# Kernel tuning notes

Hardware: AMD Instinct MI355X
Metric: run time of the kernel (lower is better)

Reference implementation:

```python
import jax, jax.numpy as jnp
import numpy as np

V, D, C, H = 32, 128, 2048, 8
B, M = 8, 2048
HD = D // H


def rms_norm(x, scale):
    # Whole-tensor (per-batch) RMS over dims (1,2), as in the source (quirky but faithful).
    Bx, Mx, Dx = x.shape
    fr = jnp.sqrt(jnp.sum(x * x, axis=(1, 2))) * (Mx * Dx) ** -0.5  # (B,)
    raw = x / fr[:, None, None]
    return scale[:Mx, :][None, :, :] * raw


def rope_tables(Mx):
    i = jnp.arange(D // 2, dtype=jnp.float32)
    # NOTE: faithful to source: exponent uses (i-1), not i.
    base = jnp.power(10000.0, -2.0 * (i - 1.0) / D)  # (D/2,)
    pos = jnp.arange(Mx, dtype=jnp.float32)
    ang = pos[:, None] * base[None, :]  # (M, D/2)
    return jnp.cos(ang), jnp.sin(ang)


def apply_rope(t, cos, sin):
    # Equivalent to bmm with the block-diagonal 2x2 rotation matrices:
    # out[2i]   =  t[2i]*cos + t[2i+1]*sin
    # out[2i+1] = -t[2i]*sin + t[2i+1]*cos
    te, to = t[..., 0::2], t[..., 1::2]
    oe = te * cos + to * sin
    oo = -te * sin + to * cos
    return jnp.stack([oe, oo], axis=-1).reshape(t.shape)


def mha(q, k, v, in_w, in_b, out_w, out_b):
    Bx, Mx, _ = q.shape
    qp = q @ in_w[:D].T + in_b[:D]
    kp = k @ in_w[D:2 * D].T + in_b[D:2 * D]
    vp = v @ in_w[2 * D:].T + in_b[2 * D:]
    qh = qp.reshape(Bx, Mx, H, HD).transpose(0, 2, 1, 3)
    kh = kp.reshape(Bx, Mx, H, HD).transpose(0, 2, 1, 3)
    vh = vp.reshape(Bx, Mx, H, HD).transpose(0, 2, 1, 3)
    scores = jnp.einsum('bhqd,bhkd->bhqk', qh, kh) / jnp.sqrt(jnp.float32(HD))
    causal = jnp.tril(jnp.ones((Mx, Mx), dtype=bool))
    scores = jnp.where(causal[None, None], scores, -jnp.inf)
    probs = jax.nn.softmax(scores, axis=-1)  # dropout=0.1 in train mode; eval here
    o = jnp.einsum('bhqk,bhkd->bhqd', probs, vh)
    o = o.transpose(0, 2, 1, 3).reshape(Bx, Mx, D)
    return o @ out_w.T + out_b


def setup_inputs():
    key = jax.random.key(0)
    ks = jax.random.split(key, 12)
    s = 0.02
    return {
        'idx': jax.random.randint(ks[0], (B, M), 0, V),
        'targets': jax.random.randint(ks[1], (B, M), 0, V),
        'emb': jax.random.normal(ks[2], (V, D), jnp.float32) * s,
        'rms_scale': jnp.ones((C, D), jnp.float32),
        'Wq': jax.random.normal(ks[3], (D, D), jnp.float32) * s,
        'Wk': jax.random.normal(ks[4], (D, D), jnp.float32) * s,
        'Wv': jax.random.normal(ks[5], (D, D), jnp.float32) * s,
        'in_proj_w': jax.random.normal(ks[6], (3 * D, D), jnp.float32) * s,
        'in_proj_b': jnp.zeros((3 * D,), jnp.float32),
        'out_proj_w': jax.random.normal(ks[7], (D, D), jnp.float32) * s,
        'out_proj_b': jnp.zeros((D,), jnp.float32),
        'lin_w': jax.random.normal(ks[8], (D, D), jnp.float32) * s,
        'lin_b': jnp.zeros((D,), jnp.float32),
        'out_w': jax.random.normal(ks[9], (V, D), jnp.float32) * s,
        'out_b': jnp.zeros((V,), jnp.float32),
    }


def reference(idx, targets, emb, rms_scale, Wq, Wk, Wv, in_proj_w, in_proj_b,
              out_proj_w, out_proj_b, lin_w, lin_b, out_w, out_b):
    x = emb[idx]                                  # (B, M, D)
    x = rms_norm(x, rms_scale)
    Q = x @ Wq.T
    K = x @ Wk.T
    Vv = x @ Wv.T
    cos, sin = rope_tables(x.shape[1])
    q_out = apply_rope(Q, cos, sin)
    k_out = apply_rope(K, cos, sin)
    v_out = apply_rope(Vv, cos, sin)              # source rotates V too (faithful)
    x = x + mha(q_out, k_out, v_out, in_proj_w, in_proj_b, out_proj_w, out_proj_b)
    x = rms_norm(x, rms_scale)
    x = x + jax.nn.relu(x @ lin_w.T + lin_b)
    logits = x @ out_w.T + out_b                  # (B, M, V)
    logp = jax.nn.log_softmax(logits, axis=-1)
    nll = -jnp.take_along_axis(logp, targets[..., None], axis=-1)[..., 0]
    loss = jnp.mean(nll)
    return logits, loss
```

## Files before the change

### kernel.cpp

```cpp
#include <hip/hip_runtime.h>
#include <hip/hip_bf16.h>
#include <math.h>

#define Vv   32
#define Dd   128
#define Hh   8
#define Bb   8
#define Mm   2048
#define BM   (Bb*Mm)
#define NEL  (BM*Dd)
#define XNS  140
#define QKS  396

typedef _Float16 half4_t __attribute__((ext_vector_type(4)));
typedef _Float16 half8_t __attribute__((ext_vector_type(8)));
typedef __fp16   fp16x2  __attribute__((ext_vector_type(2)));
typedef float    float4_t __attribute__((ext_vector_type(4)));
#define MFMA16 __builtin_amdgcn_mfma_f32_16x16x16f16

#if __has_builtin(__builtin_amdgcn_exp2f)
__device__ __forceinline__ float fexp2(float x) { return __builtin_amdgcn_exp2f(x); }
#else
__device__ __forceinline__ float fexp2(float x) { return __expf(x * 0.6931471805599453f); }
#endif

__global__ __launch_bounds__(256) void prep_kernel(const float* __restrict__ Wq,
                                                   const float* __restrict__ Wk,
                                                   const float* __restrict__ Wv,
                                                   const float* __restrict__ in_w,
                                                   const float* __restrict__ out_pw,
                                                   const float* __restrict__ lin_w,
                                                   const float* __restrict__ out_w,
                                                   _Float16* __restrict__ Wh,
                                                   float* __restrict__ cosT,
                                                   float* __restrict__ sinT) {
    int gid = blockIdx.x * 256 + threadIdx.x;
    if (gid < 135168) {
        const float* src;
        int i;
        if (gid < 131072) {
            int seg = gid >> 14; i = gid & 16383;
            src = seg == 0 ? Wq : seg == 1 ? Wk : seg == 2 ? Wv :
                  seg < 6 ? in_w + (size_t)(seg - 3) * 16384 :
                  seg == 6 ? out_pw : lin_w;
        } else { src = out_w; i = gid - 131072; }
        int tile = i >> 8, within = i & 255;
        int nt = tile >> 3, kk = tile & 7;
        int r = within >> 4, cc = within & 15;
        Wh[gid] = (_Float16)src[(nt * 16 + r) * 128 + kk * 16 + cc];
    } else {
        int rid = gid - 135168;
        int i = rid & 63, m = rid >> 6;
        float ex = -2.0f * ((float)i - 1.0f) / 128.0f;
        float basef = expf(ex * 9.210340371976184f);
        float ang = (float)m * basef;
        cosT[rid] = cosf(ang);
        sinT[rid] = sinf(ang);
    }
}

__global__ __launch_bounds__(256) void gather_sumsq_kernel(const int* __restrict__ idx,
                                                           const float* __restrict__ emb,
                                                           _Float16* __restrict__ Xh,
                                                           float* __restrict__ partials) {
    int gid = blockIdx.x * 256 + threadIdx.x;
    int token = gid >> 5, t4 = gid & 31;
    float4 x = *(const float4*)(emb + (size_t)idx[token] * 128 + t4 * 4);
    half4_t o;
    o[0] = (_Float16)x.x; o[1] = (_Float16)x.y; o[2] = (_Float16)x.z; o[3] = (_Float16)x.w;
    *(half4_t*)(Xh + (size_t)gid * 4) = o;
    float v = x.x * x.x + x.y * x.y + x.z * x.z + x.w * x.w;
    #pragma unroll
    for (int off = 32; off; off >>= 1) v += __shfl_xor(v, off);
    __shared__ float wsum[4];
    int lane = threadIdx.x & 63, wave = threadIdx.x >> 6;
    if (lane == 0) wsum[wave] = v;
    __syncthreads();
    if (threadIdx.x == 0) partials[blockIdx.x] = wsum[0] + wsum[1] + wsum[2] + wsum[3];
}

__global__ __launch_bounds__(256) void normscale_f_kernel(const float* __restrict__ X,
                                                          const float* __restrict__ scale,
                                                          const float* __restrict__ part2,
                                                          _Float16* __restrict__ outh) {
    int gid = blockIdx.x * 256 + threadIdx.x;
    int b = gid >> 16;
    float pv = part2[b * 64 + (threadIdx.x & 63)];
    #pragma unroll
    for (int off = 32; off; off >>= 1) pv += __shfl_xor(pv, off);
    float iv = 512.0f / sqrtf(pv);
    const float* sp = scale + (size_t)((gid >> 5) & 2047) * 128 + (gid & 31) * 4;
    float4 s4 = *(const float4*)sp;
    float4 x = *(const float4*)(X + (size_t)gid * 4);
    half4_t o;
    o[0] = (_Float16)(x.x * iv * s4.x);
    o[1] = (_Float16)(x.y * iv * s4.y);
    o[2] = (_Float16)(x.z * iv * s4.z);
    o[3] = (_Float16)(x.w * iv * s4.w);
    *(half4_t*)(outh + (size_t)gid * 4) = o;
}

__global__ __launch_bounds__(256) void gemm_qkvproj_kernel(const _Float16* __restrict__ xh,
                                                           const float* __restrict__ scale,
                                                           const float* __restrict__ part1,
                                                           const _Float16* __restrict__ Whqkv,
                                                           const _Float16* __restrict__ Whin,
                                                           const float* __restrict__ in_b,
                                                           const float* __restrict__ cosT,
                                                           const float* __restrict__ sinT,
                                                           _Float16* __restrict__ xnh,
                                                           _Float16* __restrict__ Qp,
                                                           _Float16* __restrict__ Kp,
                                                           _Float16* __restrict__ Vp) {
    __shared__ _Float16 xn[32 * XNS];
    __shared__ _Float16 qkv[32 * QKS];
    __shared__ float wsum0[4];
    int tid = threadIdx.x;
    int row0 = blockIdx.x * 32;
    {
        float v = part1[(row0 >> 11) * 256 + tid];
        #pragma unroll
        for (int off = 32; off; off >>= 1) v += __shfl_xor(v, off);
        if ((tid & 63) == 0) wsum0[tid >> 6] = v;
    }
    __syncthreads();
    float iv = 512.0f / sqrtf(wsum0[0] + wsum0[1] + wsum0[2] + wsum0[3]);
    {
        #pragma unroll
        for (int it = 0; it < 2; it++) {
            int idx = tid + it * 256;
            int rw = idx >> 4, c8 = (idx & 15) * 8;
            int m = (row0 + rw) & (Mm - 1);
            half8_t x8 = *(const half8_t*)(xh + (size_t)(row0 + rw) * 128 + c8);
            const float* sp = scale + (size_t)m * 128 + c8;
            float4 s0 = *(const float4*)sp;
            float4 s1 = *(const float4*)(sp + 4);
            half8_t o8;
            o8[0] = (_Float16)((float)x8[0] * iv * s0.x);
            o8[1] = (_Float16)((float)x8[1] * iv * s0.y);
            o8[2] = (_Float16)((float)x8[2] * iv * s0.z);
            o8[3] = (_Float16)((float)x8[3] * iv * s0.w);
            o8[4] = (_Float16)((float)x8[4] * iv * s1.x);
            o8[5] = (_Float16)((float)x8[5] * iv * s1.y);
            o8[6] = (_Float16)((float)x8[6] * iv * s1.z);
            o8[7] = (_Float16)((float)x8[7] * iv * s1.w);
            *(half8_t*)(xn + rw * XNS + c8) = o8;
            *(half8_t*)(xnh + (size_t)(row0 + rw) * 128 + c8) = o8;
        }
    }
    __syncthreads();
    int wave = tid >> 6, lane = tid & 63;
    int r = lane & 15, c = lane >> 4;
    int lofs = r * 16 + 4 * c;
    int nb = wave * 96;
    int nb16 = wave * 6;
    {
        half4_t af[2][8];
        #pragma unroll
        for (int rt = 0; rt < 2; rt++)
            #pragma unroll
            for (int kk = 0; kk < 8; kk++)
                af[rt][kk] = *(const half4_t*)(xn + (rt * 16 + r) * XNS + kk * 16 + 4 * c);
        float4_t acc[2][6];
        #pragma unroll
        for (int rt = 0; rt < 2; rt++)
            #pragma unroll
            for (int t = 0; t < 6; t++) acc[rt][t] = (float4_t){0.f, 0.f, 0.f, 0.f};
        #pragma unroll
        for (int kk = 0; kk < 8; kk++) {
            half4_t wf[6];
            #pragma unroll
            for (int t = 0; t < 6; t++)
                wf[t] = *(const half4_t*)(Whqkv + ((nb16 + t) * 8 + kk) * 256 + lofs);
            #pragma unroll
            for (int t = 0; t < 6; t++) {
                acc[0][t] = MFMA16(af[0][kk], wf[t], acc[0][t], 0, 0, 0);
                acc[1][t] = MFMA16(af[1][kk], wf[t], acc[1][t], 0, 0, 0);
            }
        }
        #pragma unroll
        for (int rt = 0; rt < 2; rt++) {
            #pragma unroll
            for (int t = 0; t < 6; t++) {
                int n = nb + t * 16 + r;
                int ci = (n & 127) >> 1;
                #pragma unroll
                for (int reg = 0; reg < 4; reg++) {
                    int m2 = (row0 + rt * 16 + 4 * c + reg) & (Mm - 1);
                    float v = acc[rt][t][reg];
                    float vp = __shfl_xor(v, 1);
                    float cs = cosT[m2 * 64 + ci], sn = sinT[m2 * 64 + ci];
                    v = (n & 1) ? (-vp * sn + v * cs) : (v * cs + vp * sn);
                    qkv[(rt * 16 + 4 * c + reg) * QKS + n] = (_Float16)v;
                }
            }
        }
    }
    __syncthreads();
    {
        int seg_lo = nb >> 7;
        int seg_hi = (nb + 80) >> 7;
        half4_t aql[2][8], aqh[2][8];
        #pragma unroll
        for (int rt = 0; rt < 2; rt++)
            #pragma unroll
            for (int kk = 0; kk < 8; kk++) {
                aql[rt][kk] = *(const half4_t*)(qkv + (rt * 16 + r) * QKS + seg_lo * 128 + kk * 16 + 4 * c);
                aqh[rt][kk] = *(const half4_t*)(qkv + (rt * 16 + r) * QKS + seg_hi * 128 + kk * 16 + 4 * c);
            }
        float4_t acc[2][6];
        #pragma unroll
        for (int rt = 0; rt < 2; rt++)
            #pragma unroll
            for (int t = 0; t < 6; t++) acc[rt][t] = (float4_t){0.f, 0.f, 0.f, 0.f};
        #pragma unroll
        for (int kk = 0; kk < 8; kk++) {
            half4_t wf[6];
            #pragma unroll
            for (int t = 0; t < 6; t++) {
                int colg = nb + t * 16;
                int seg = colg >> 7;
                int ntl = (colg & 127) >> 4;
                wf[t] = *(const half4_t*)(Whin + ((seg * 8 + ntl) * 8 + kk) * 256 + lofs);
            }
            #pragma unroll
            for (int t = 0; t < 6; t++) {
                int seg = (nb + t * 16) >> 7;
                acc[0][t] = MFMA16(seg == seg_lo ? aql[0][kk] : aqh[0][kk], wf[t], acc[0][t], 0, 0, 0);
                acc[1][t] = MFMA16(seg == seg_lo ? aql[1][kk] : aqh[1][kk], wf[t], acc[1][t], 0, 0, 0);
            }
        }
        int bb = row0 >> 11;
        #pragma unroll
        for (int rt = 0; rt < 2; rt++) {
            int t16 = ((row0 + rt * 16) & 2047) >> 4;
            #pragma unroll
            for (int t = 0; t < 6; t++) {
                int colg = nb + t * 16;
                int seg = colg >> 7;
                int h = (colg & 127) >> 4;
                size_t tb = ((size_t)(bb * 8 + h) * 128 + t16) * 256;
                float bv = in_b[colg + r];
                _Float16* dst = seg == 0 ? Qp : seg == 1 ? Kp : Vp;
                #pragma unroll
                for (int reg = 0; reg < 4; reg++) {
                    float v = acc[rt][t][reg] + bv;
                    int key = 4 * c + reg;
                    if (seg < 2) dst[tb + key * 16 + r] = (_Float16)v;
                    else         dst[tb + r * 16 + key] = (_Float16)v;
                }
            }
        }
    }
}

__global__ __launch_bounds__(256) void gemm_ep1_kernel(const _Float16* __restrict__ Oh,
                                                       const _Float16* __restrict__ W6,
                                                       const float* __restrict__ bias,
                                                       const _Float16* __restrict__ xnh,
                                                       float* __restrict__ xres,
                                                       float* __restrict__ partials) {
    __shared__ _Float16 At[32 * XNS];
    int tid = threadIdx.x;
    int row0 = blockIdx.x * 32;
    #pragma unroll
    for (int it = 0; it < 2; it++) {
        int idx = tid + it * 256;
        int rw = idx >> 4, c8 = (idx & 15) * 8;
        *(half8_t*)(At + rw * XNS + c8) = *(const half8_t*)(Oh + (size_t)(row0 + rw) * 128 + c8);
    }
    __syncthreads();
    int wave = tid >> 6, lane = tid & 63;
    int r = lane & 15, c = lane >> 4;
    int lofs = r * 16 + 4 * c;
    int n0 = wave * 32;
    half4_t af[2][8];
    #pragma unroll
    for (int rt = 0; rt < 2; rt++)
        #pragma unroll
        for (int kk = 0; kk < 8; kk++)
            af[rt][kk] = *(const half4_t*)(At + (rt * 16 + r) * XNS + kk * 16 + 4 * c);
    float4_t acc[2][2];
    #pragma unroll
    for (int rt = 0; rt < 2; rt++) {
        acc[rt][0] = (float4_t){0.f, 0.f, 0.f, 0.f};
        acc[rt][1] = (float4_t){0.f, 0.f, 0.f, 0.f};
    }
    #pragma unroll
    for (int kk = 0; kk < 8; kk++) {
        half4_t wf[2];
        wf[0] = *(const half4_t*)(W6 + ((wave * 2 + 0) * 8 + kk) * 256 + lofs);
        wf[1] = *(const half4_t*)(W6 + ((wave * 2 + 1) * 8 + kk) * 256 + lofs);
        #pragma unroll
        for (int t = 0; t < 2; t++) {
            acc[0][t] = MFMA16(af[0][kk], wf[t], acc[0][t], 0, 0, 0);
            acc[1][t] = MFMA16(af[1][kk], wf[t], acc[1][t], 0, 0, 0);
        }
    }
    float lssq = 0.f;
    #pragma unroll
    for (int rt = 0; rt < 2; rt++) {
        #pragma unroll
        for (int t = 0; t < 2; t++) {
            int n = n0 + t * 16 + r;
            float bv = bias[n];
            #pragma unroll
            for (int reg = 0; reg < 4; reg++) {
                int row = row0 + rt * 16 + 4 * c + reg;
                float v = acc[rt][t][reg] + bv + (float)xnh[(size_t)row * 128 + n];
                lssq += v * v;
                xres[(size_t)row * 128 + n] = v;
            }
        }
    }
    #pragma unroll
    for (int off = 32; off; off >>= 1) lssq += __shfl_xor(lssq, off);
    __shared__ float wsum[4];
    if (lane == 0) wsum[wave] = lssq;
    __syncthreads();
    if (tid == 0) partials[blockIdx.x] = wsum[0] + wsum[1] + wsum[2] + wsum[3];
}

__global__ __launch_bounds__(256) void gemm_ep2_kernel(const _Float16* __restrict__ Ah,
                                                       const _Float16* __restrict__ W7,
                                                       const float* __restrict__ bias,
                                                       const float* __restrict__ xres,
                                                       _Float16* __restrict__ ffoh) {
    __shared__ _Float16 At[32 * XNS];
    int tid = threadIdx.x;
    int row0 = blockIdx.x * 32;
    #pragma unroll
    for (int it = 0; it < 2; it++) {
        int idx = tid + it * 256;
        int rw = idx >> 4, c8 = (idx & 15) * 8;
        *(half8_t*)(At + rw * XNS + c8) = *(const half8_t*)(Ah + (size_t)(row0 + rw) * 128 + c8);
    }
    __syncthreads();
    int wave = tid >> 6, lane = tid & 63;
    int r = lane & 15, c = lane >> 4;
    int lofs = r * 16 + 4 * c;
    int n0 = wave * 32;
    half4_t af[2][8];
    #pragma unroll
    for (int rt = 0; rt < 2; rt++)
        #pragma unroll
        for (int kk = 0; kk < 8; kk++)
            af[rt][kk] = *(const half4_t*)(At + (rt * 16 + r) * XNS + kk * 16 + 4 * c);
    float4_t acc[2][2];
    #pragma unroll
    for (int rt = 0; rt < 2; rt++) {
        acc[rt][0] = (float4_t){0.f, 0.f, 0.f, 0.f};
        acc[rt][1] = (float4_t){0.f, 0.f, 0.f, 0.f};
    }
    #pragma unroll
    for (int kk = 0; kk < 8; kk++) {
        half4_t wf[2];
        wf[0] = *(const half4_t*)(W7 + ((wave * 2 + 0) * 8 + kk) * 256 + lofs);
        wf[1] = *(const half4_t*)(W7 + ((wave * 2 + 1) * 8 + kk) * 256 + lofs);
        #pragma unroll
        for (int t = 0; t < 2; t++) {
            acc[0][t] = MFMA16(af[0][kk], wf[t], acc[0][t], 0, 0, 0);
            acc[1][t] = MFMA16(af[1][kk], wf[t], acc[1][t], 0, 0, 0);
        }
    }
    #pragma unroll
    for (int rt = 0; rt < 2; rt++) {
        #pragma unroll
        for (int t = 0; t < 2; t++) {
            int n = n0 + t * 16 + r;
            float bv = bias[n];
            #pragma unroll
            for (int reg = 0; reg < 4; reg++) {
                int row = row0 + rt * 16 + 4 * c + reg;
                float v = fmaxf(acc[rt][t][reg] + bv, 0.f) + xres[(size_t)row * 128 + n];
                ffoh[(size_t)row * 128 + n] = (_Float16)v;
            }
        }
    }
}

__device__ __forceinline__ half4_t attn_exps(float4_t st, float& ls) {
    float p0 = fexp2(st[0]), p1 = fexp2(st[1]);
    float p2 = fexp2(st[2]), p3 = fexp2(st[3]);
    fp16x2 lo = __builtin_amdgcn_cvt_pkrtz(p0, p1);
    fp16x2 hi = __builtin_amdgcn_cvt_pkrtz(p2, p3);
#if __has_builtin(__builtin_amdgcn_fdot2)
    fp16x2 one2 = {(__fp16)1.0f, (__fp16)1.0f};
    ls = __builtin_amdgcn_fdot2(lo, one2, ls, false);
    ls = __builtin_amdgcn_fdot2(hi, one2, ls, false);
#else
    ls += (p0 + p1) + (p2 + p3);
#endif
    half4_t pf;
    pf[0] = (_Float16)lo[0]; pf[1] = (_Float16)lo[1];
    pf[2] = (_Float16)hi[0]; pf[3] = (_Float16)hi[1];
    return pf;
}
__device__ __forceinline__ half4_t attn_exps_masked(float4_t st, float& ls, int r, int c) {
    float p0 = (4 * c + 0 <= r) ? fexp2(st[0]) : 0.f;
    float p1 = (4 * c + 1 <= r) ? fexp2(st[1]) : 0.f;
    float p2 = (4 * c + 2 <= r) ? fexp2(st[2]) : 0.f;
    float p3 = (4 * c + 3 <= r) ? fexp2(st[3]) : 0.f;
    fp16x2 lo = __builtin_amdgcn_cvt_pkrtz(p0, p1);
    fp16x2 hi = __builtin_amdgcn_cvt_pkrtz(p2, p3);
#if __has_builtin(__builtin_amdgcn_fdot2)
    fp16x2 one2 = {(__fp16)1.0f, (__fp16)1.0f};
    ls = __builtin_amdgcn_fdot2(lo, one2, ls, false);
    ls = __builtin_amdgcn_fdot2(hi, one2, ls, false);
#else
    ls += (p0 + p1) + (p2 + p3);
#endif
    half4_t pf;
    pf[0] = (_Float16)lo[0]; pf[1] = (_Float16)lo[1];
    pf[2] = (_Float16)hi[0]; pf[3] = (_Float16)hi[1];
    return pf;
}

__global__ __launch_bounds__(256) void attn_kernel(const _Float16* __restrict__ Qp,
                                                   const _Float16* __restrict__ Kp,
                                                   const _Float16* __restrict__ Vp,
                                                   _Float16* __restrict__ Oh) {
    int wave = threadIdx.x >> 6, lane = threadIdx.x & 63;
    int wid = blockIdx.x * 4 + wave;
    int qa = wid & 63, bh = wid >> 6, qb = 127 - qa;
    int r = lane & 15, c = lane >> 4;
    int lofs = r * 16 + 4 * c;
    const _Float16* Kb = Kp + (size_t)bh * 32768 + lofs;
    const _Float16* Vb = Vp + (size_t)bh * 32768 + lofs;
    const _Float16* Qb = Qp + (size_t)bh * 32768 + lofs;
    half4_t qfa = *(const half4_t*)(Qb + qa * 256);
    half4_t qfb = *(const half4_t*)(Qb + qb * 256);
    const _Float16 qscale = (_Float16)0.36067376f;
    qfa *= qscale;
    qfb *= qscale;
    float4_t zero = {0.f, 0.f, 0.f, 0.f};
    float4_t oa = zero, ob = zero;
    float lsa = 0.f, lsb = 0.f;
    int nt = qb + 1;

    half4_t k0 = *(const half4_t*)(Kb);
    half4_t v0 = *(const half4_t*)(Vb);
    half4_t k1 = *(const half4_t*)(Kb + 256);
    half4_t v1 = *(const half4_t*)(Vb + 256);
    for (int kt = 0; kt < nt; kt += 2) {
        half4_t kn0 = k0, vn0 = v0, kn1 = k1, vn1 = v1;
        if (kt + 2 < nt) {
            kn0 = *(const half4_t*)(Kb + (size_t)(kt + 2) * 256);
            vn0 = *(const half4_t*)(Vb + (size_t)(kt + 2) * 256);
        }
        if (kt + 3 < nt) {
            kn1 = *(const half4_t*)(Kb + (size_t)(kt + 3) * 256);
            vn1 = *(const half4_t*)(Vb + (size_t)(kt + 3) * 256);
        }
        {
            float4_t sb = MFMA16(k0, qfb, zero, 0, 0, 0);
            if (kt <= qa) {
                float4_t sa = MFMA16(k0, qfa, zero, 0, 0, 0);
                half4_t pa = (kt == qa) ? attn_exps_masked(sa, lsa, r, c) : attn_exps(sa, lsa);
                oa = MFMA16(pa, v0, oa, 0, 0, 0);
            }
            half4_t pb = (kt == qb) ? attn_exps_masked(sb, lsb, r, c) : attn_exps(sb, lsb);
            ob = MFMA16(pb, v0, ob, 0, 0, 0);
        }
        if (kt + 1 < nt) {
            float4_t sb = MFMA16(k1, qfb, zero, 0, 0, 0);
            if (kt + 1 <= qa) {
                float4_t sa = MFMA16(k1, qfa, zero, 0, 0, 0);
                half4_t pa = (kt + 1 == qa) ? attn_exps_masked(sa, lsa, r, c) : attn_exps(sa, lsa);
                oa = MFMA16(pa, v1, oa, 0, 0, 0);
            }
            half4_t pb = (kt + 1 == qb) ? attn_exps_masked(sb, lsb, r, c) : attn_exps(sb, lsb);
            ob = MFMA16(pb, v1, ob, 0, 0, 0);
        }
        k0 = kn0; v0 = vn0; k1 = kn1; v1 = vn1;
    }
    lsa += __shfl_xor(lsa, 16); lsa += __shfl_xor(lsa, 32);
    lsb += __shfl_xor(lsb, 16); lsb += __shfl_xor(lsb, 32);
    int b = bh >> 3, h = bh & 7;
    #pragma unroll
    for (int reg = 0; reg < 4; reg++) {
        float la = __shfl(lsa, 4 * c + reg);
        float lb = __shfl(lsb, 4 * c + reg);
        Oh[(size_t)(b * Mm + qa * 16 + 4 * c + reg) * 128 + h * 16 + r] = (_Float16)(oa[reg] / la);
        Oh[(size_t)(b * Mm + qb * 16 + 4 * c + reg) * 128 + h * 16 + r] = (_Float16)(ob[reg] / lb);
    }
}

__global__ __launch_bounds__(256) void logits_loss_kernel(const _Float16* __restrict__ Xh,
                                                          const _Float16* __restrict__ Wo16,
                                                          const float* __restrict__ bo,
                                                          const int* __restrict__ targets,
                                                          float* __restrict__ logits,
                                                          float* __restrict__ nllBuf) {
    __shared__ _Float16 At[64 * XNS];
    int tid = threadIdx.x;
    int rowb = blockIdx.x * 64;
    #pragma unroll
    for (int it = 0; it < 4; it++) {
        int idx = tid + it * 256;
        int rw = idx >> 4, c8 = (idx & 15) * 8;
        *(half8_t*)(At + rw * XNS + c8) = *(const half8_t*)(Xh + (size_t)(rowb + rw) * 128 + c8);
    }
    __syncthreads();
    int wave = tid >> 6, lane = tid & 63;
    int r = lane & 15, c = lane >> 4;
    int lofs = r * 16 + 4 * c;
    int row0 = rowb + wave * 16;
    half4_t af[8];
    #pragma unroll
    for (int kk = 0; kk < 8; kk++)
        af[kk] = *(const half4_t*)(At + (wave * 16 + r) * XNS + kk * 16 + 4 * c);
    float4_t acc[2];
    acc[0] = (float4_t){0.f, 0.f, 0.f, 0.f};
    acc[1] = (float4_t){0.f, 0.f, 0.f, 0.f};
    #pragma unroll
    for (int kk = 0; kk < 8; kk++) {
        #pragma unroll
        for (int t = 0; t < 2; t++) {
            half4_t wf = *(const half4_t*)(Wo16 + (t * 8 + kk) * 256 + lofs);
            acc[t] = MFMA16(af[kk], wf, acc[t], 0, 0, 0);
        }
    }
    float b0 = bo[r], b1 = bo[r + 16];
    #pragma unroll
    for (int reg = 0; reg < 4; reg++) {
        int row = row0 + 4 * c + reg;
        float l0 = acc[0][reg] + b0;
        float l1 = acc[1][reg] + b1;
        logits[(size_t)row * 32 + r] = l0;
        logits[(size_t)row * 32 + 16 + r] = l1;
        float mx = fmaxf(l0, l1);
        #pragma unroll
        for (int off = 8; off; off >>= 1) mx = fmaxf(mx, __shfl_xor(mx, off));
        float se = __expf(l0 - mx) + __expf(l1 - mx);
        #pragma unroll
        for (int off = 8; off; off >>= 1) se += __shfl_xor(se, off);
        int tgt = targets[row];
        float sel = (tgt & 16) ? l1 : l0;
        float tval = __shfl(sel, (lane & 48) | (tgt & 15));
        if (r == 0) nllBuf[row] = logf(se) + mx - tval;
    }
}

__global__ __launch_bounds__(256) void loss_reduce_kernel(const float* __restrict__ nllBuf,
                                                          float* __restrict__ out) {
    int t = threadIdx.x;
    double s = 0.0;
    #pragma unroll
    for (int i = 0; i < 64; i++) s += (double)nllBuf[t * 64 + i];
    __shared__ double sh[256];
    sh[t] = s;
    __syncthreads();
    for (int off = 128; off; off >>= 1) {
        if (t < off) sh[t] += sh[t + off];
        __syncthreads();
    }
    if (t == 0) out[0] = (float)(sh[0] * (1.0 / (double)BM));
}

extern "C" void kernel_launch(void* const* d_in, const int* in_sizes, int n_in,
                              void* d_out, int out_size, void* d_ws, size_t ws_size,
                              hipStream_t stream) {
    const int*   idx       = (const int*)d_in[0];
    const int*   targets   = (const int*)d_in[1];
    const float* emb       = (const float*)d_in[2];
    const float* rms_scale = (const float*)d_in[3];
    const float* Wq        = (const float*)d_in[4];
    const float* Wk        = (const float*)d_in[5];
    const float* Wv        = (const float*)d_in[6];
    const float* in_w      = (const float*)d_in[7];
    const float* in_b      = (const float*)d_in[8];
    const float* out_pw    = (const float*)d_in[9];
    const float* out_pb    = (const float*)d_in[10];
    const float* lin_w     = (const float*)d_in[11];
    const float* lin_b     = (const float*)d_in[12];
    const float* out_w     = (const float*)d_in[13];
    const float* out_b     = (const float*)d_in[14];
    float* out = (float*)d_out;

    char* base = (char*)d_ws;
    const size_t MB = 1024 * 1024;
    _Float16* xh16  = (_Float16*)base;
    _Float16* xnh   = (_Float16*)(base + 4 * MB);
    _Float16* Oh    = (_Float16*)(base + 8 * MB);
    _Float16* x2nh  = (_Float16*)(base + 12 * MB);
    _Float16* ffoh  = (_Float16*)(base + 16 * MB);
    _Float16* Qp    = (_Float16*)(base + 20 * MB);
    _Float16* Kp    = (_Float16*)(base + 24 * MB);
    _Float16* Vp    = (_Float16*)(base + 28 * MB);
    float*    xres  = (float*)(base + 32 * MB);
    float*    cosT  = (float*)(base + 40 * MB);
    float*    sinT  = cosT + Mm * 64;
    float*    part1 = sinT + Mm * 64;
    float*    part2 = part1 + 2048;
    _Float16* Wh    = (_Float16*)(part2 + 512);
    float*    nllBuf = (float*)(Wh + 135168);

    prep_kernel<<<1040, 256, 0, stream>>>(Wq, Wk, Wv, in_w, out_pw, lin_w, out_w, Wh, cosT, sinT);
    gather_sumsq_kernel<<<NEL / 1024, 256, 0, stream>>>(idx, emb, xh16, part1);

    gemm_qkvproj_kernel<<<BM / 32, 256, 0, stream>>>(xh16, rms_scale, part1,
                                                     Wh, Wh + 3 * 16384, in_b,
                                                     cosT, sinT, xnh, Qp, Kp, Vp);

    attn_kernel<<<64 * 64 / 4, 256, 0, stream>>>(Qp, Kp, Vp, Oh);

    gemm_ep1_kernel<<<BM / 32, 256, 0, stream>>>(Oh, Wh + 6 * 16384, out_pb, xnh, xres, part2);
    normscale_f_kernel<<<NEL / 1024, 256, 0, stream>>>(xres, rms_scale, part2, x2nh);
    gemm_ep2_kernel<<<BM / 32, 256, 0, stream>>>(x2nh, Wh + 7 * 16384, lin_b, xres, ffoh);

    logits_loss_kernel<<<BM / 64, 256, 0, stream>>>(ffoh, Wh + 131072, out_b, targets, out, nllBuf);
    loss_reduce_kernel<<<1, 256, 0, stream>>>(nllBuf, out + (size_t)BM * Vv);
}
```

Measured before the change: 181.4 us.

## Split attention key range across two waves and merge via shared memory

Each query-tile pair is now handled by two waves that take alternating key tiles, and the partial outputs and row sums are combined through shared memory before the final normalization. This doubles the grid and halves the serial loop length per wave, which raises parallelism and latency hiding in the attention kernel. The loop is also restructured into separate unmasked, diagonal and tail phases, and the register prefetch double-buffering is dropped. The row sum now uses fp32 adds instead of packed fp16 dot instructions, and the change adds a block barrier plus shared-memory traffic.

```diff
diff --git a/kernel.cpp b/kernel.cpp
--- a/kernel.cpp
+++ b/kernel.cpp
@@ -382,15 +382,9 @@
 __device__ __forceinline__ half4_t attn_exps(float4_t st, float& ls) {
     float p0 = fexp2(st[0]), p1 = fexp2(st[1]);
     float p2 = fexp2(st[2]), p3 = fexp2(st[3]);
+    ls += (p0 + p1) + (p2 + p3);
     fp16x2 lo = __builtin_amdgcn_cvt_pkrtz(p0, p1);
     fp16x2 hi = __builtin_amdgcn_cvt_pkrtz(p2, p3);
-#if __has_builtin(__builtin_amdgcn_fdot2)
-    fp16x2 one2 = {(__fp16)1.0f, (__fp16)1.0f};
-    ls = __builtin_amdgcn_fdot2(lo, one2, ls, false);
-    ls = __builtin_amdgcn_fdot2(hi, one2, ls, false);
-#else
-    ls += (p0 + p1) + (p2 + p3);
-#endif
     half4_t pf;
     pf[0] = (_Float16)lo[0]; pf[1] = (_Float16)lo[1];
     pf[2] = (_Float16)hi[0]; pf[3] = (_Float16)hi[1];
@@ -401,15 +395,9 @@
     float p1 = (4 * c + 1 <= r) ? fexp2(st[1]) : 0.f;
     float p2 = (4 * c + 2 <= r) ? fexp2(st[2]) : 0.f;
     float p3 = (4 * c + 3 <= r) ? fexp2(st[3]) : 0.f;
+    ls += (p0 + p1) + (p2 + p3);
     fp16x2 lo = __builtin_amdgcn_cvt_pkrtz(p0, p1);
     fp16x2 hi = __builtin_amdgcn_cvt_pkrtz(p2, p3);
-#if __has_builtin(__builtin_amdgcn_fdot2)
-    fp16x2 one2 = {(__fp16)1.0f, (__fp16)1.0f};
-    ls = __builtin_amdgcn_fdot2(lo, one2, ls, false);
-    ls = __builtin_amdgcn_fdot2(hi, one2, ls, false);
-#else
-    ls += (p0 + p1) + (p2 + p3);
-#endif
     half4_t pf;
     pf[0] = (_Float16)lo[0]; pf[1] = (_Float16)lo[1];
     pf[2] = (_Float16)hi[0]; pf[3] = (_Float16)hi[1];
@@ -420,9 +408,11 @@
                                                    const _Float16* __restrict__ Kp,
                                                    const _Float16* __restrict__ Vp,
                                                    _Float16* __restrict__ Oh) {
+    __shared__ float mrg[2][10][64];
     int wave = threadIdx.x >> 6, lane = threadIdx.x & 63;
-    int wid = blockIdx.x * 4 + wave;
-    int qa = wid & 63, bh = wid >> 6, qb = 127 - qa;
+    int pair = blockIdx.x * 2 + (wave >> 1);
+    int split = wave & 1;
+    int qa = pair & 63, bh = pair >> 6, qb = 127 - qa;
     int r = lane & 15, c = lane >> 4;
     int lofs = r * 16 + 4 * c;
     const _Float16* Kb = Kp + (size_t)bh * 32768 + lofs;
@@ -436,53 +426,74 @@
     float4_t zero = {0.f, 0.f, 0.f, 0.f};
     float4_t oa = zero, ob = zero;
     float lsa = 0.f, lsb = 0.f;
-    int nt = qb + 1;
-
-    half4_t k0 = *(const half4_t*)(Kb);
-    half4_t v0 = *(const half4_t*)(Vb);
-    half4_t k1 = *(const half4_t*)(Kb + 256);
-    half4_t v1 = *(const half4_t*)(Vb + 256);
-    for (int kt = 0; kt < nt; kt += 2) {
-        half4_t kn0 = k0, vn0 = v0, kn1 = k1, vn1 = v1;
-        if (kt + 2 < nt) {
-            kn0 = *(const half4_t*)(Kb + (size_t)(kt + 2) * 256);
-            vn0 = *(const half4_t*)(Vb + (size_t)(kt + 2) * 256);
-        }
-        if (kt + 3 < nt) {
-            kn1 = *(const half4_t*)(Kb + (size_t)(kt + 3) * 256);
-            vn1 = *(const half4_t*)(Vb + (size_t)(kt + 3) * 256);
-        }
-        {
+
+    for (int kt = split; kt < qa; kt += 2) {
+        half4_t k0 = *(const half4_t*)(Kb + (size_t)kt * 256);
+        half4_t v0 = *(const half4_t*)(Vb + (size_t)kt * 256);
+        float4_t sa = MFMA16(k0, qfa, zero, 0, 0, 0);
+        float4_t sb = MFMA16(k0, qfb, zero, 0, 0, 0);
+        half4_t pa = attn_exps(sa, lsa);
+        half4_t pb = attn_exps(sb, lsb);
+        oa = MFMA16(pa, v0, oa, 0, 0, 0);
+        ob = MFMA16(pb, v0, ob, 0, 0, 0);
+    }
+    if ((qa & 1) == split) {
+        half4_t k0 = *(const half4_t*)(Kb + (size_t)qa * 256);
+        half4_t v0 = *(const half4_t*)(Vb + (size_t)qa * 256);
+        float4_t sa = MFMA16(k0, qfa, zero, 0, 0, 0);
+        float4_t sb = MFMA16(k0, qfb, zero, 0, 0, 0);
+        half4_t pa = attn_exps_masked(sa, lsa, r, c);
+        half4_t pb = attn_exps(sb, lsb);
+        oa = MFMA16(pa, v0, oa, 0, 0, 0);
+        ob = MFMA16(pb, v0, ob, 0, 0, 0);
+    }
+    {
+        int s = qa + 1;
+        if ((s & 1) != split) s++;
+        for (int kt = s; kt < qb; kt += 2) {
+            half4_t k0 = *(const half4_t*)(Kb + (size_t)kt * 256);
+            half4_t v0 = *(const half4_t*)(Vb + (size_t)kt * 256);
             float4_t sb = MFMA16(k0, qfb, zero, 0, 0, 0);
-            if (kt <= qa) {
-                float4_t sa = MFMA16(k0, qfa, zero, 0, 0, 0);
-                half4_t pa = (kt == qa) ? attn_exps_masked(sa, lsa, r, c) : attn_exps(sa, lsa);
-                oa = MFMA16(pa, v0, oa, 0, 0, 0);
-            }
-            half4_t pb = (kt == qb) ? attn_exps_masked(sb, lsb, r, c) : attn_exps(sb, lsb);
+            half4_t pb = attn_exps(sb, lsb);
             ob = MFMA16(pb, v0, ob, 0, 0, 0);
         }
-        if (kt + 1 < nt) {
-            float4_t sb = MFMA16(k1, qfb, zero, 0, 0, 0);
-            if (kt + 1 <= qa) {
-                float4_t sa = MFMA16(k1, qfa, zero, 0, 0, 0);
-                half4_t pa = (kt + 1 == qa) ? attn_exps_masked(sa, lsa, r, c) : attn_exps(sa, lsa);
-                oa = MFMA16(pa, v1, oa, 0, 0, 0);
-            }
-            half4_t pb = (kt + 1 == qb) ? attn_exps_masked(sb, lsb, r, c) : attn_exps(sb, lsb);
-            ob = MFMA16(pb, v1, ob, 0, 0, 0);
-        }
-        k0 = kn0; v0 = vn0; k1 = kn1; v1 = vn1;
-    }
-    lsa += __shfl_xor(lsa, 16); lsa += __shfl_xor(lsa, 32);
-    lsb += __shfl_xor(lsb, 16); lsb += __shfl_xor(lsb, 32);
-    int b = bh >> 3, h = bh & 7;
-    #pragma unroll
-    for (int reg = 0; reg < 4; reg++) {
-        float la = __shfl(lsa, 4 * c + reg);
-        float lb = __shfl(lsb, 4 * c + reg);
-        Oh[(size_t)(b * Mm + qa * 16 + 4 * c + reg) * 128 + h * 16 + r] = (_Float16)(oa[reg] / la);
-        Oh[(size_t)(b * Mm + qb * 16 + 4 * c + reg) * 128 + h * 16 + r] = (_Float16)(ob[reg] / lb);
+    }
+    if ((qb & 1) == split) {
+        half4_t k0 = *(const half4_t*)(Kb + (size_t)qb * 256);
+        half4_t v0 = *(const half4_t*)(Vb + (size_t)qb * 256);
+        float4_t sb = MFMA16(k0, qfb, zero, 0, 0, 0);
+        half4_t pb = attn_exps_masked(sb, lsb, r, c);
+        ob = MFMA16(pb, v0, ob, 0, 0, 0);
+    }
+    int pib = wave >> 1;
+    if (split == 1) {
+        #pragma unroll
+        for (int i = 0; i < 4; i++) {
+            mrg[pib][i][lane] = oa[i];
+            mrg[pib][4 + i][lane] = ob[i];
+        }
+        mrg[pib][8][lane] = lsa;
+        mrg[pib][9][lane] = lsb;
+    }
+    __syncthreads();
+    if (split == 0) {
+        #pragma unroll
+        for (int i = 0; i < 4; i++) {
+            oa[i] += mrg[pib][i][lane];
+            ob[i] += mrg[pib][4 + i][lane];
+        }
+        lsa += mrg[pib][8][lane];
+        lsb += mrg[pib][9][lane];
+        lsa += __shfl_xor(lsa, 16); lsa += __shfl_xor(lsa, 32);
+        lsb += __shfl_xor(lsb, 16); lsb += __shfl_xor(lsb, 32);
+        int b = bh >> 3, h = bh & 7;
+        #pragma unroll
+        for (int reg = 0; reg < 4; reg++) {
+            float la = __shfl(lsa, 4 * c + reg);
+            float lb = __shfl(lsb, 4 * c + reg);
+            Oh[(size_t)(b * Mm + qa * 16 + 4 * c + reg) * 128 + h * 16 + r] = (_Float16)(oa[reg] / la);
+            Oh[(size_t)(b * Mm + qb * 16 + 4 * c + reg) * 128 + h * 16 + r] = (_Float16)(ob[reg] / lb);
+        }
     }
 }
 
@@ -603,7 +614,7 @@
                                                      Wh, Wh + 3 * 16384, in_b,
                                                      cosT, sinT, xnh, Qp, Kp, Vp);
 
-    attn_kernel<<<64 * 64 / 4, 256, 0, stream>>>(Qp, Kp, Vp, Oh);
+    attn_kernel<<<4096 / 2, 256, 0, stream>>>(Qp, Kp, Vp, Oh);
 
     gemm_ep1_kernel<<<BM / 32, 256, 0, stream>>>(Oh, Wh + 6 * 16384, out_pb, xnh, xres, part2);
     normscale_f_kernel<<<NEL / 1024, 256, 0, stream>>>(xres, rms_scale, part2, x2nh);
```

Measured after the change: 169.0 us. -6.8%, faster.
